# Kernel tuning notes

Measured on AMD Instinct MI355X. Metric: run time of the kernel, lower is better.

The kernel has to match this reference:

```python
import jax, jax.numpy as jnp
import numpy as np

N_NODES = 50000
N_EDGES = 500000
NODE_IN = 128
EDGE_IN = 64
HID = 128
OUT = 1


def _linear_params(key, fan_in, fan_out):
    # torch nn.Linear default init: U(-1/sqrt(fan_in), 1/sqrt(fan_in))
    kw, kb = jax.random.split(key)
    bound = 1.0 / np.sqrt(fan_in)
    W = jax.random.uniform(kw, (fan_in, fan_out), jnp.float32, -bound, bound)
    b = jax.random.uniform(kb, (fan_out,), jnp.float32, -bound, bound)
    return W, b


def setup_inputs() -> dict:
    key = jax.random.key(0)
    ks = jax.random.split(key, 8)
    x = jax.random.normal(ks[0], (N_NODES, NODE_IN), jnp.float32)
    edge_index = jax.random.randint(ks[1], (2, N_EDGES), 0, N_NODES, jnp.int64)
    edge_attr = jax.random.normal(ks[2], (N_EDGES, EDGE_IN), jnp.float32)
    Wn, bn = _linear_params(ks[3], NODE_IN, HID)
    We, be = _linear_params(ks[4], EDGE_IN, HID)
    W1, b1 = _linear_params(ks[5], HID * 3, HID * 4)
    W2, b2 = _linear_params(ks[6], HID * 4, HID * 2)
    W3, b3 = _linear_params(ks[7], HID * 2, OUT)
    return {
        "x": x, "edge_index": edge_index, "edge_attr": edge_attr,
        "Wn": Wn, "bn": bn, "We": We, "be": be,
        "W1": W1, "b1": b1, "W2": W2, "b2": b2, "W3": W3, "b3": b3,
    }


def reference(x, edge_index, edge_attr, Wn, bn, We, be, W1, b1, W2, b2, W3, b3):
    src, dst = edge_index[0], edge_index[1]
    node_f = jax.nn.relu(x @ Wn + bn)          # [N, H]
    edge_f = jax.nn.relu(edge_attr @ We + be)  # [E, H]
    combined = jnp.concatenate([node_f[src], node_f[dst], edge_f], axis=1)  # [E, 3H]
    h = jax.nn.relu(combined @ W1 + b1)        # [E, 4H]
    h = jax.nn.relu(h @ W2 + b2)               # [E, 2H]
    return h @ W3 + b3                          # [E, OUT]
```

## Files before the change

### kernel.cpp

```cpp
#include <hip/hip_runtime.h>
#include <hip/hip_bf16.h>
#include <stdint.h>

#define N_NODES 50000
#define N_EDGES 500000
#define NODE_IN 128
#define EDGE_IN 64
#define HID 128
#define K_H1 384
#define N_H1 512
#define N_H2 256

#define EPB 64

typedef short s8v __attribute__((ext_vector_type(8)));
typedef float f4v __attribute__((ext_vector_type(4)));

__device__ __forceinline__ unsigned int pk_bf16(float a, float b) {
    union { __hip_bfloat162 h; unsigned int u; } c;
    c.h = __float22bfloat162_rn(float2{a, b});
    return c.u;
}

__device__ __forceinline__ s8v load_a_f32(const float* __restrict__ base, int row, int ld, int koff) {
    const float4* p = (const float4*)(base + row * ld + koff);
    float4 x0 = p[0];
    float4 x1 = p[1];
    union { s8v v; unsigned int u[4]; } r;
    r.u[0] = pk_bf16(x0.x, x0.y);
    r.u[1] = pk_bf16(x0.z, x0.w);
    r.u[2] = pk_bf16(x1.x, x1.y);
    r.u[3] = pk_bf16(x1.z, x1.w);
    return r.v;
}

__device__ __forceinline__ void pack_one(const float* __restrict__ src, unsigned short* __restrict__ dst,
                                         int idx, int N) {
    int j = idx & 7;
    int lane = (idx >> 3) & 63;
    int rest = idx >> 9;
    int NT = N >> 4;
    int nt = rest % NT;
    int kb = rest / NT;
    int n = nt * 16 + (lane & 15);
    int k = kb * 32 + ((lane >> 4) << 3) + j;
    union { __hip_bfloat16 h; unsigned short s; } c;
    c.h = __float2bfloat16(src[k * N + n]);
    dst[idx] = c.s;
}

#define WN_ELEMS (NODE_IN * HID)
#define WE_ELEMS (EDGE_IN * HID)
#define W1_ELEMS (K_H1 * N_H1)
#define W2_ELEMS (N_H1 * N_H2)
#define PACK_TOTAL (WN_ELEMS + WE_ELEMS + W1_ELEMS + W2_ELEMS)

__global__ void pack_all(const float* __restrict__ Wn, const float* __restrict__ We,
                         const float* __restrict__ W1, const float* __restrict__ W2,
                         unsigned short* __restrict__ Wnp, unsigned short* __restrict__ Wep,
                         unsigned short* __restrict__ W1p, unsigned short* __restrict__ W2p) {
    int idx = blockIdx.x * blockDim.x + threadIdx.x;
    if (idx >= PACK_TOTAL) return;
    if (idx < WN_ELEMS) { pack_one(Wn, Wnp, idx, HID); return; }
    idx -= WN_ELEMS;
    if (idx < WE_ELEMS) { pack_one(We, Wep, idx, HID); return; }
    idx -= WE_ELEMS;
    if (idx < W1_ELEMS) { pack_one(W1, W1p, idx, N_H1); return; }
    idx -= W1_ELEMS;
    pack_one(W2, W2p, idx, N_H2);
}

__global__ __launch_bounds__(256, 4) void node_feat_kernel(
    const float* __restrict__ x, const unsigned short* __restrict__ Wnp,
    const float* __restrict__ bn, unsigned short* __restrict__ node_f)
{
    int tid = threadIdx.x;
    int wave = tid >> 6, lane = tid & 63;
    int lm = lane & 15, quad = lane >> 4;
    int row0 = blockIdx.x * 64;
    int node = row0 + wave * 16 + lm;
    int nodec = node < N_NODES ? node : N_NODES - 1;

    f4v zero = {0.f, 0.f, 0.f, 0.f};
    f4v acc[8];
    #pragma unroll
    for (int mt = 0; mt < 8; ++mt) acc[mt] = zero;

    for (int kb = 0; kb < 4; ++kb) {
        s8v b = load_a_f32(x, nodec, NODE_IN, kb * 32 + quad * 8);
        #pragma unroll
        for (int mt = 0; mt < 8; ++mt) {
            s8v a = *(const s8v*)(Wnp + (((kb * 8 + mt) * 64 + lane) << 3));
            acc[mt] = __builtin_amdgcn_mfma_f32_16x16x32_bf16(a, b, acc[mt], 0, 0, 0);
        }
    }

    if (node < N_NODES) {
        #pragma unroll
        for (int mt = 0; mt < 8; ++mt) {
            float4 bv = *(const float4*)(bn + mt * 16 + quad * 4);
            uint2 pk;
            pk.x = pk_bf16(fmaxf(acc[mt][0] + bv.x, 0.f), fmaxf(acc[mt][1] + bv.y, 0.f));
            pk.y = pk_bf16(fmaxf(acc[mt][2] + bv.z, 0.f), fmaxf(acc[mt][3] + bv.w, 0.f));
            *(uint2*)(node_f + node * HID + mt * 16 + quad * 4) = pk;
        }
    }
}

#define CSTR 392
#define H1STR 520

__global__ __launch_bounds__(512, 4) void fused_edge_kernel(
    const int* __restrict__ edge_index, const float* __restrict__ edge_attr,
    const unsigned short* __restrict__ node_f,
    const unsigned short* __restrict__ Wep, const float* __restrict__ be,
    const unsigned short* __restrict__ W1p, const float* __restrict__ b1,
    const unsigned short* __restrict__ W2p, const float* __restrict__ b2,
    const float* __restrict__ W3, const float* __restrict__ b3,
    float* __restrict__ out)
{
    __shared__ __align__(16) unsigned short smem[EPB * H1STR];
    __shared__ float out_lds[EPB];

    int tid = threadIdx.x;
    int wave = tid >> 6, lane = tid & 63;
    int lm = lane & 15, quad = lane >> 4;
    int e0 = blockIdx.x * EPB;

    if (tid < EPB) out_lds[tid] = 0.f;

    int gi = tid >> 3, gp = tid & 7;
    uint4 gs0, gs1, gd0, gd1;
    {
        int e = e0 + gi;
        int ec = e < N_EDGES ? e : N_EDGES - 1;
        int s = edge_index[ec];
        int d = edge_index[N_EDGES + ec];
        const uint4* ps = (const uint4*)(node_f + s * HID + gp * 16);
        const uint4* pd = (const uint4*)(node_f + d * HID + gp * 16);
        gs0 = ps[0]; gs1 = ps[1];
        gd0 = pd[0]; gd1 = pd[1];
    }

    {
        int nt = wave & 3;
        int mbase = (wave >> 2) * 4;
        int erow = e0 + nt * 16 + lm;
        if (erow >= N_EDGES) erow = N_EDGES - 1;

        f4v zero = {0.f, 0.f, 0.f, 0.f};
        f4v acc[4];
        #pragma unroll
        for (int t = 0; t < 4; ++t) acc[t] = zero;

        for (int kb = 0; kb < 2; ++kb) {
            s8v b = load_a_f32(edge_attr, erow, EDGE_IN, kb * 32 + quad * 8);
            #pragma unroll
            for (int t = 0; t < 4; ++t) {
                s8v a = *(const s8v*)(Wep + (((kb * 8 + mbase + t) * 64 + lane) << 3));
                acc[t] = __builtin_amdgcn_mfma_f32_16x16x32_bf16(a, b, acc[t], 0, 0, 0);
            }
        }
        {
            uint4* cs = (uint4*)(smem + gi * CSTR + gp * 16);
            uint4* cd = (uint4*)(smem + gi * CSTR + 128 + gp * 16);
            cs[0] = gs0; cs[1] = gs1;
            cd[0] = gd0; cd[1] = gd1;
        }
        int edge = nt * 16 + lm;
        #pragma unroll
        for (int t = 0; t < 4; ++t) {
            int col = (mbase + t) * 16 + quad * 4;
            float4 bv = *(const float4*)(be + col);
            uint2 pk;
            pk.x = pk_bf16(fmaxf(acc[t][0] + bv.x, 0.f), fmaxf(acc[t][1] + bv.y, 0.f));
            pk.y = pk_bf16(fmaxf(acc[t][2] + bv.z, 0.f), fmaxf(acc[t][3] + bv.w, 0.f));
            *(uint2*)(smem + edge * CSTR + 256 + col) = pk;
        }
    }
    __syncthreads();

    f4v zero = {0.f, 0.f, 0.f, 0.f};
    f4v acc1[4][4];
    #pragma unroll
    for (int t = 0; t < 4; ++t)
        #pragma unroll
        for (int nt = 0; nt < 4; ++nt) acc1[t][nt] = zero;

    for (int kb = 0; kb < 12; ++kb) {
        s8v bfr[4];
        #pragma unroll
        for (int nt = 0; nt < 4; ++nt)
            bfr[nt] = *(const s8v*)(smem + (nt * 16 + lm) * CSTR + kb * 32 + quad * 8);
        s8v afr[4];
        #pragma unroll
        for (int t = 0; t < 4; ++t)
            afr[t] = *(const s8v*)(W1p + (((kb * 32 + wave * 4 + t) * 64 + lane) << 3));
        #pragma unroll
        for (int t = 0; t < 4; ++t)
            #pragma unroll
            for (int nt = 0; nt < 4; ++nt)
                acc1[t][nt] = __builtin_amdgcn_mfma_f32_16x16x32_bf16(afr[t], bfr[nt], acc1[t][nt], 0, 0, 0);
    }
    __syncthreads();

    #pragma unroll
    for (int t = 0; t < 4; ++t) {
        int col = (wave * 4 + t) * 16 + quad * 4;
        float4 bv = *(const float4*)(b1 + col);
        #pragma unroll
        for (int nt = 0; nt < 4; ++nt) {
            int edge = nt * 16 + lm;
            uint2 pk;
            pk.x = pk_bf16(fmaxf(acc1[t][nt][0] + bv.x, 0.f), fmaxf(acc1[t][nt][1] + bv.y, 0.f));
            pk.y = pk_bf16(fmaxf(acc1[t][nt][2] + bv.z, 0.f), fmaxf(acc1[t][nt][3] + bv.w, 0.f));
            *(uint2*)(smem + edge * H1STR + col) = pk;
        }
    }
    __syncthreads();

    f4v acc2[2][4];
    #pragma unroll
    for (int t = 0; t < 2; ++t)
        #pragma unroll
        for (int nt = 0; nt < 4; ++nt) acc2[t][nt] = zero;

    for (int kb = 0; kb < 16; ++kb) {
        s8v bfr[4];
        #pragma unroll
        for (int nt = 0; nt < 4; ++nt)
            bfr[nt] = *(const s8v*)(smem + (nt * 16 + lm) * H1STR + kb * 32 + quad * 8);
        s8v afr[2];
        #pragma unroll
        for (int t = 0; t < 2; ++t)
            afr[t] = *(const s8v*)(W2p + (((kb * 16 + wave * 2 + t) * 64 + lane) << 3));
        #pragma unroll
        for (int t = 0; t < 2; ++t)
            #pragma unroll
            for (int nt = 0; nt < 4; ++nt)
                acc2[t][nt] = __builtin_amdgcn_mfma_f32_16x16x32_bf16(afr[t], bfr[nt], acc2[t][nt], 0, 0, 0);
    }

    {
        float4 b2v[2], w3v[2];
        #pragma unroll
        for (int t = 0; t < 2; ++t) {
            int col = (wave * 2 + t) * 16 + quad * 4;
            b2v[t] = *(const float4*)(b2 + col);
            w3v[t] = *(const float4*)(W3 + col);
        }
        #pragma unroll
        for (int nt = 0; nt < 4; ++nt) {
            float p = 0.f;
            #pragma unroll
            for (int t = 0; t < 2; ++t) {
                p += fmaxf(acc2[t][nt][0] + b2v[t].x, 0.f) * w3v[t].x;
                p += fmaxf(acc2[t][nt][1] + b2v[t].y, 0.f) * w3v[t].y;
                p += fmaxf(acc2[t][nt][2] + b2v[t].z, 0.f) * w3v[t].z;
                p += fmaxf(acc2[t][nt][3] + b2v[t].w, 0.f) * w3v[t].w;
            }
            p += __shfl_xor(p, 16);
            p += __shfl_xor(p, 32);
            if (quad == 0)
                atomicAdd(&out_lds[nt * 16 + lm], p);
        }
    }
    __syncthreads();

    if (tid < EPB) {
        int e = e0 + tid;
        if (e < N_EDGES) out[e] = out_lds[tid] + b3[0];
    }
}

extern "C" void kernel_launch(void* const* d_in, const int* in_sizes, int n_in,
                              void* d_out, int out_size, void* d_ws, size_t ws_size,
                              hipStream_t stream)
{
    const float* x          = (const float*)d_in[0];
    const int*   edge_index = (const int*)d_in[1];
    const float* edge_attr  = (const float*)d_in[2];
    const float* Wn = (const float*)d_in[3];
    const float* bn = (const float*)d_in[4];
    const float* We = (const float*)d_in[5];
    const float* be = (const float*)d_in[6];
    const float* W1 = (const float*)d_in[7];
    const float* b1 = (const float*)d_in[8];
    const float* W2 = (const float*)d_in[9];
    const float* b2 = (const float*)d_in[10];
    const float* W3 = (const float*)d_in[11];
    const float* b3 = (const float*)d_in[12];
    float* out = (float*)d_out;

    char* ws = (char*)d_ws;
    unsigned short* node_f = (unsigned short*)ws;
    unsigned short* Wnp = (unsigned short*)(ws + 12800000);
    unsigned short* Wep = (unsigned short*)(ws + 12832768);
    unsigned short* W1p = (unsigned short*)(ws + 12849152);
    unsigned short* W2p = (unsigned short*)(ws + 13242368);

    pack_all<<<(PACK_TOTAL + 255) / 256, 256, 0, stream>>>(Wn, We, W1, W2, Wnp, Wep, W1p, W2p);

    node_feat_kernel<<<(N_NODES + 63) / 64, 256, 0, stream>>>(x, Wnp, bn, node_f);

    fused_edge_kernel<<<(N_EDGES + EPB - 1) / EPB, 512, 0, stream>>>(
        edge_index, edge_attr, node_f, Wep, be, W1p, b1, W2p, b2, W3, b3, out);
}
```

Before: 604.7 us.

## Double-buffer W1/W2 fragment loads in registers with explicit waitcnt pipelining

The two MFMA GEMM loops in the fused edge kernel now prefetch the next k-step's weight fragments from global memory into alternating register sets while the current step's MFMAs run. Explicit s_waitcnt and sched_barrier calls control when loads must have landed. The point is to hide global-load latency of the packed weights behind matrix math instead of stalling each iteration. The last iteration prefetches past the end of each weight buffer, so the workspace is reordered to keep those over-reads inside allocated memory. This adds register pressure and relies on hand-written wait counts staying correct.

```diff
diff --git a/kernel.cpp b/kernel.cpp
--- a/kernel.cpp
+++ b/kernel.cpp
@@ -178,6 +178,12 @@
             *(uint2*)(smem + edge * CSTR + 256 + col) = pk;
         }
     }
+
+    const unsigned short* wb1 = W1p + (((wave * 4) * 64 + lane) << 3);
+    s8v aev[4], aod[4];
+    #pragma unroll
+    for (int t = 0; t < 4; ++t) aev[t] = *(const s8v*)(wb1 + t * 512);
+
     __syncthreads();
 
     f4v zero = {0.f, 0.f, 0.f, 0.f};
@@ -187,20 +193,41 @@
         #pragma unroll
         for (int nt = 0; nt < 4; ++nt) acc1[t][nt] = zero;
 
-    for (int kb = 0; kb < 12; ++kb) {
+    {
+        const unsigned short* brp = smem + lm * CSTR + quad * 8;
+        const unsigned short* wnext = wb1 + 16384;
+
         s8v bfr[4];
-        #pragma unroll
-        for (int nt = 0; nt < 4; ++nt)
-            bfr[nt] = *(const s8v*)(smem + (nt * 16 + lm) * CSTR + kb * 32 + quad * 8);
-        s8v afr[4];
-        #pragma unroll
-        for (int t = 0; t < 4; ++t)
-            afr[t] = *(const s8v*)(W1p + (((kb * 32 + wave * 4 + t) * 64 + lane) << 3));
-        #pragma unroll
-        for (int t = 0; t < 4; ++t)
+        #pragma unroll 1
+        for (int kb = 0; kb < 12; kb += 2) {
+            #pragma unroll
+            for (int t = 0; t < 4; ++t) aod[t] = *(const s8v*)(wnext + t * 512);
+            wnext += 16384;
             #pragma unroll
             for (int nt = 0; nt < 4; ++nt)
-                acc1[t][nt] = __builtin_amdgcn_mfma_f32_16x16x32_bf16(afr[t], bfr[nt], acc1[t][nt], 0, 0, 0);
+                bfr[nt] = *(const s8v*)(brp + nt * (16 * CSTR));
+            asm volatile("s_waitcnt vmcnt(4) lgkmcnt(0)" ::: "memory");
+            __builtin_amdgcn_sched_barrier(0);
+            #pragma unroll
+            for (int t = 0; t < 4; ++t)
+                #pragma unroll
+                for (int nt = 0; nt < 4; ++nt)
+                    acc1[t][nt] = __builtin_amdgcn_mfma_f32_16x16x32_bf16(aev[t], bfr[nt], acc1[t][nt], 0, 0, 0);
+            #pragma unroll
+            for (int t = 0; t < 4; ++t) aev[t] = *(const s8v*)(wnext + t * 512);
+            wnext += 16384;
+            #pragma unroll
+            for (int nt = 0; nt < 4; ++nt)
+                bfr[nt] = *(const s8v*)(brp + 32 + nt * (16 * CSTR));
+            asm volatile("s_waitcnt vmcnt(4) lgkmcnt(0)" ::: "memory");
+            __builtin_amdgcn_sched_barrier(0);
+            #pragma unroll
+            for (int t = 0; t < 4; ++t)
+                #pragma unroll
+                for (int nt = 0; nt < 4; ++nt)
+                    acc1[t][nt] = __builtin_amdgcn_mfma_f32_16x16x32_bf16(aod[t], bfr[nt], acc1[t][nt], 0, 0, 0);
+            brp += 64;
+        }
     }
     __syncthreads();
 
@@ -217,6 +244,12 @@
             *(uint2*)(smem + edge * H1STR + col) = pk;
         }
     }
+
+    const unsigned short* wb2 = W2p + (((wave * 2) * 64 + lane) << 3);
+    s8v a3ev[2], a3od[2];
+    a3ev[0] = *(const s8v*)(wb2);
+    a3ev[1] = *(const s8v*)(wb2 + 512);
+
     __syncthreads();
 
     f4v acc2[2][4];
@@ -225,20 +258,41 @@
         #pragma unroll
         for (int nt = 0; nt < 4; ++nt) acc2[t][nt] = zero;
 
-    for (int kb = 0; kb < 16; ++kb) {
+    {
+        const unsigned short* hrp = smem + lm * H1STR + quad * 8;
+        const unsigned short* wnext = wb2 + 8192;
+
         s8v bfr[4];
-        #pragma unroll
-        for (int nt = 0; nt < 4; ++nt)
-            bfr[nt] = *(const s8v*)(smem + (nt * 16 + lm) * H1STR + kb * 32 + quad * 8);
-        s8v afr[2];
-        #pragma unroll
-        for (int t = 0; t < 2; ++t)
-            afr[t] = *(const s8v*)(W2p + (((kb * 16 + wave * 2 + t) * 64 + lane) << 3));
-        #pragma unroll
-        for (int t = 0; t < 2; ++t)
+        #pragma unroll 1
+        for (int kb = 0; kb < 16; kb += 2) {
+            a3od[0] = *(const s8v*)(wnext);
+            a3od[1] = *(const s8v*)(wnext + 512);
+            wnext += 8192;
             #pragma unroll
             for (int nt = 0; nt < 4; ++nt)
-                acc2[t][nt] = __builtin_amdgcn_mfma_f32_16x16x32_bf16(afr[t], bfr[nt], acc2[t][nt], 0, 0, 0);
+                bfr[nt] = *(const s8v*)(hrp + nt * (16 * H1STR));
+            asm volatile("s_waitcnt vmcnt(2) lgkmcnt(0)" ::: "memory");
+            __builtin_amdgcn_sched_barrier(0);
+            #pragma unroll
+            for (int t = 0; t < 2; ++t)
+                #pragma unroll
+                for (int nt = 0; nt < 4; ++nt)
+                    acc2[t][nt] = __builtin_amdgcn_mfma_f32_16x16x32_bf16(a3ev[t], bfr[nt], acc2[t][nt], 0, 0, 0);
+            a3ev[0] = *(const s8v*)(wnext);
+            a3ev[1] = *(const s8v*)(wnext + 512);
+            wnext += 8192;
+            #pragma unroll
+            for (int nt = 0; nt < 4; ++nt)
+                bfr[nt] = *(const s8v*)(hrp + 32 + nt * (16 * H1STR));
+            asm volatile("s_waitcnt vmcnt(2) lgkmcnt(0)" ::: "memory");
+            __builtin_amdgcn_sched_barrier(0);
+            #pragma unroll
+            for (int t = 0; t < 2; ++t)
+                #pragma unroll
+                for (int nt = 0; nt < 4; ++nt)
+                    acc2[t][nt] = __builtin_amdgcn_mfma_f32_16x16x32_bf16(a3od[t], bfr[nt], acc2[t][nt], 0, 0, 0);
+            hrp += 64;
+        }
     }
 
     {
@@ -294,10 +348,10 @@
 
     char* ws = (char*)d_ws;
     unsigned short* node_f = (unsigned short*)ws;
-    unsigned short* Wnp = (unsigned short*)(ws + 12800000);
-    unsigned short* Wep = (unsigned short*)(ws + 12832768);
-    unsigned short* W1p = (unsigned short*)(ws + 12849152);
-    unsigned short* W2p = (unsigned short*)(ws + 13242368);
+    unsigned short* W1p = (unsigned short*)(ws + 12800000);
+    unsigned short* W2p = (unsigned short*)(ws + 13193216);
+    unsigned short* Wnp = (unsigned short*)(ws + 13455360);
+    unsigned short* Wep = (unsigned short*)(ws + 13488128);
 
     pack_all<<<(PACK_TOTAL + 255) / 256, 256, 0, stream>>>(Wn, We, W1, W2, Wnp, Wep, W1p, W2p);
 
```

After: 500.3 us. 1.21x faster.

## Switch edge MLP GEMMs to 32x32x16 MFMA with software-pipelined operand loads

Applied to the files above, without the earlier changes.

Repacks W1 and W2 into a 32x32 MFMA fragment layout and rewrites the two big edge-MLP GEMMs to use mfma_f32_32x32x16_bf16 tiles. The K loops are double-buffered: the next weight and LDS fragments are loaded while the current MFMAs run, using explicit waitcnt and sched_barrier. The first weight fragments are prefetched before each __syncthreads. The intent is fewer fragment loads per FLOP and better hiding of global and LDS latency. The price is hand-managed wait counts that are fragile, plus a different register footprint.

```diff
diff --git a/kernel.cpp b/kernel.cpp
--- a/kernel.cpp
+++ b/kernel.cpp
@@ -15,6 +15,7 @@
 
 typedef short s8v __attribute__((ext_vector_type(8)));
 typedef float f4v __attribute__((ext_vector_type(4)));
+typedef float f16v __attribute__((ext_vector_type(16)));
 
 __device__ __forceinline__ unsigned int pk_bf16(float a, float b) {
     union { __hip_bfloat162 h; unsigned int u; } c;
@@ -49,6 +50,21 @@
     dst[idx] = c.s;
 }
 
+__device__ __forceinline__ void pack_one32(const float* __restrict__ src, unsigned short* __restrict__ dst,
+                                           int idx, int N) {
+    int j = idx & 7;
+    int lane = (idx >> 3) & 63;
+    int rest = idx >> 9;
+    int NT = N >> 5;
+    int nt = rest % NT;
+    int ks = rest / NT;
+    int n = nt * 32 + (lane & 31);
+    int k = ks * 16 + ((lane >> 5) << 3) + j;
+    union { __hip_bfloat16 h; unsigned short s; } c;
+    c.h = __float2bfloat16(src[k * N + n]);
+    dst[idx] = c.s;
+}
+
 #define WN_ELEMS (NODE_IN * HID)
 #define WE_ELEMS (EDGE_IN * HID)
 #define W1_ELEMS (K_H1 * N_H1)
@@ -65,9 +81,9 @@
     idx -= WN_ELEMS;
     if (idx < WE_ELEMS) { pack_one(We, Wep, idx, HID); return; }
     idx -= WE_ELEMS;
-    if (idx < W1_ELEMS) { pack_one(W1, W1p, idx, N_H1); return; }
+    if (idx < W1_ELEMS) { pack_one32(W1, W1p, idx, N_H1); return; }
     idx -= W1_ELEMS;
-    pack_one(W2, W2p, idx, N_H2);
+    pack_one32(W2, W2p, idx, N_H2);
 }
 
 __global__ __launch_bounds__(256, 4) void node_feat_kernel(
@@ -125,6 +141,7 @@
     int tid = threadIdx.x;
     int wave = tid >> 6, lane = tid & 63;
     int lm = lane & 15, quad = lane >> 4;
+    int e32 = lane & 31, hi = lane >> 5;
     int e0 = blockIdx.x * EPB;
 
     if (tid < EPB) out_lds[tid] = 0.f;
@@ -148,10 +165,10 @@
         int erow = e0 + nt * 16 + lm;
         if (erow >= N_EDGES) erow = N_EDGES - 1;
 
-        f4v zero = {0.f, 0.f, 0.f, 0.f};
+        f4v zero4 = {0.f, 0.f, 0.f, 0.f};
         f4v acc[4];
         #pragma unroll
-        for (int t = 0; t < 4; ++t) acc[t] = zero;
+        for (int t = 0; t < 4; ++t) acc[t] = zero4;
 
         for (int kb = 0; kb < 2; ++kb) {
             s8v b = load_a_f32(edge_attr, erow, EDGE_IN, kb * 32 + quad * 8);
@@ -178,91 +195,151 @@
             *(uint2*)(smem + edge * CSTR + 256 + col) = pk;
         }
     }
+
+    const unsigned short* wb1 = W1p + (((wave * 2) * 64 + lane) << 3);
+    s8v aev[2], aod[2];
+    aev[0] = *(const s8v*)(wb1);
+    aev[1] = *(const s8v*)(wb1 + 512);
+
     __syncthreads();
 
-    f4v zero = {0.f, 0.f, 0.f, 0.f};
-    f4v acc1[4][4];
-    #pragma unroll
-    for (int t = 0; t < 4; ++t)
-        #pragma unroll
-        for (int nt = 0; nt < 4; ++nt) acc1[t][nt] = zero;
-
-    for (int kb = 0; kb < 12; ++kb) {
-        s8v bfr[4];
-        #pragma unroll
-        for (int nt = 0; nt < 4; ++nt)
-            bfr[nt] = *(const s8v*)(smem + (nt * 16 + lm) * CSTR + kb * 32 + quad * 8);
-        s8v afr[4];
-        #pragma unroll
-        for (int t = 0; t < 4; ++t)
-            afr[t] = *(const s8v*)(W1p + (((kb * 32 + wave * 4 + t) * 64 + lane) << 3));
-        #pragma unroll
-        for (int t = 0; t < 4; ++t)
-            #pragma unroll
-            for (int nt = 0; nt < 4; ++nt)
-                acc1[t][nt] = __builtin_amdgcn_mfma_f32_16x16x32_bf16(afr[t], bfr[nt], acc1[t][nt], 0, 0, 0);
-    }
-    __syncthreads();
-
-    #pragma unroll
-    for (int t = 0; t < 4; ++t) {
-        int col = (wave * 4 + t) * 16 + quad * 4;
-        float4 bv = *(const float4*)(b1 + col);
-        #pragma unroll
-        for (int nt = 0; nt < 4; ++nt) {
-            int edge = nt * 16 + lm;
-            uint2 pk;
-            pk.x = pk_bf16(fmaxf(acc1[t][nt][0] + bv.x, 0.f), fmaxf(acc1[t][nt][1] + bv.y, 0.f));
-            pk.y = pk_bf16(fmaxf(acc1[t][nt][2] + bv.z, 0.f), fmaxf(acc1[t][nt][3] + bv.w, 0.f));
-            *(uint2*)(smem + edge * H1STR + col) = pk;
-        }
-    }
-    __syncthreads();
-
-    f4v acc2[2][4];
+    f16v acc1[2][2];
     #pragma unroll
     for (int t = 0; t < 2; ++t)
         #pragma unroll
-        for (int nt = 0; nt < 4; ++nt) acc2[t][nt] = zero;
-
-    for (int kb = 0; kb < 16; ++kb) {
-        s8v bfr[4];
-        #pragma unroll
-        for (int nt = 0; nt < 4; ++nt)
-            bfr[nt] = *(const s8v*)(smem + (nt * 16 + lm) * H1STR + kb * 32 + quad * 8);
-        s8v afr[2];
-        #pragma unroll
-        for (int t = 0; t < 2; ++t)
-            afr[t] = *(const s8v*)(W2p + (((kb * 16 + wave * 2 + t) * 64 + lane) << 3));
-        #pragma unroll
-        for (int t = 0; t < 2; ++t)
-            #pragma unroll
-            for (int nt = 0; nt < 4; ++nt)
-                acc2[t][nt] = __builtin_amdgcn_mfma_f32_16x16x32_bf16(afr[t], bfr[nt], acc2[t][nt], 0, 0, 0);
-    }
-
-    {
-        float4 b2v[2], w3v[2];
+        for (int n = 0; n < 2; ++n)
+            acc1[t][n] = (f16v){0.f,0.f,0.f,0.f,0.f,0.f,0.f,0.f,
+                                0.f,0.f,0.f,0.f,0.f,0.f,0.f,0.f};
+
+    {
+        const unsigned short* brp = smem + e32 * CSTR + hi * 8;
+        s8v bev[2], bod[2];
+        bev[0] = *(const s8v*)(brp);
+        bev[1] = *(const s8v*)(brp + 32 * CSTR);
+
+        const unsigned short* wnx = wb1 + 8192;
+        const unsigned short* bnx = brp + 16;
+
+        #pragma unroll 1
+        for (int ks = 0; ks < 24; ks += 2) {
+            aod[0] = *(const s8v*)(wnx);
+            aod[1] = *(const s8v*)(wnx + 512);
+            wnx += 8192;
+            bod[0] = *(const s8v*)(bnx);
+            bod[1] = *(const s8v*)(bnx + 32 * CSTR);
+            bnx += 16;
+            asm volatile("s_waitcnt vmcnt(2) lgkmcnt(2)" ::: "memory");
+            __builtin_amdgcn_sched_barrier(0);
+            #pragma unroll
+            for (int t = 0; t < 2; ++t)
+                #pragma unroll
+                for (int n = 0; n < 2; ++n)
+                    acc1[t][n] = __builtin_amdgcn_mfma_f32_32x32x16_bf16(aev[t], bev[n], acc1[t][n], 0, 0, 0);
+            aev[0] = *(const s8v*)(wnx);
+            aev[1] = *(const s8v*)(wnx + 512);
+            wnx += 8192;
+            bev[0] = *(const s8v*)(bnx);
+            bev[1] = *(const s8v*)(bnx + 32 * CSTR);
+            bnx += 16;
+            asm volatile("s_waitcnt vmcnt(2) lgkmcnt(2)" ::: "memory");
+            __builtin_amdgcn_sched_barrier(0);
+            #pragma unroll
+            for (int t = 0; t < 2; ++t)
+                #pragma unroll
+                for (int n = 0; n < 2; ++n)
+                    acc1[t][n] = __builtin_amdgcn_mfma_f32_32x32x16_bf16(aod[t], bod[n], acc1[t][n], 0, 0, 0);
+        }
+    }
+    __syncthreads();
+
+    {
         #pragma unroll
         for (int t = 0; t < 2; ++t) {
-            int col = (wave * 2 + t) * 16 + quad * 4;
-            b2v[t] = *(const float4*)(b2 + col);
-            w3v[t] = *(const float4*)(W3 + col);
-        }
-        #pragma unroll
-        for (int nt = 0; nt < 4; ++nt) {
-            float p = 0.f;
-            #pragma unroll
-            for (int t = 0; t < 2; ++t) {
-                p += fmaxf(acc2[t][nt][0] + b2v[t].x, 0.f) * w3v[t].x;
-                p += fmaxf(acc2[t][nt][1] + b2v[t].y, 0.f) * w3v[t].y;
-                p += fmaxf(acc2[t][nt][2] + b2v[t].z, 0.f) * w3v[t].z;
-                p += fmaxf(acc2[t][nt][3] + b2v[t].w, 0.f) * w3v[t].w;
+            int mb = (wave * 2 + t) * 32 + 4 * hi;
+            #pragma unroll
+            for (int g = 0; g < 4; ++g) {
+                float4 bv = *(const float4*)(b1 + mb + g * 8);
+                #pragma unroll
+                for (int n = 0; n < 2; ++n) {
+                    int edge = n * 32 + e32;
+                    uint2 pk;
+                    pk.x = pk_bf16(fmaxf(acc1[t][n][4 * g + 0] + bv.x, 0.f),
+                                   fmaxf(acc1[t][n][4 * g + 1] + bv.y, 0.f));
+                    pk.y = pk_bf16(fmaxf(acc1[t][n][4 * g + 2] + bv.z, 0.f),
+                                   fmaxf(acc1[t][n][4 * g + 3] + bv.w, 0.f));
+                    *(uint2*)(smem + edge * H1STR + mb + g * 8) = pk;
+                }
             }
-            p += __shfl_xor(p, 16);
-            p += __shfl_xor(p, 32);
-            if (quad == 0)
-                atomicAdd(&out_lds[nt * 16 + lm], p);
+        }
+    }
+
+    const unsigned short* wb2 = W2p + ((wave * 64 + lane) << 3);
+    s8v a3ev, a3od;
+    a3ev = *(const s8v*)(wb2);
+
+    __syncthreads();
+
+    f16v acc2[2];
+    #pragma unroll
+    for (int n = 0; n < 2; ++n)
+        acc2[n] = (f16v){0.f,0.f,0.f,0.f,0.f,0.f,0.f,0.f,
+                         0.f,0.f,0.f,0.f,0.f,0.f,0.f,0.f};
+
+    {
+        const unsigned short* hrp = smem + e32 * H1STR + hi * 8;
+        s8v bev[2], bod[2];
+        bev[0] = *(const s8v*)(hrp);
+        bev[1] = *(const s8v*)(hrp + 32 * H1STR);
+
+        const unsigned short* wnx = wb2 + 4096;
+        const unsigned short* bnx = hrp + 16;
+
+        #pragma unroll 1
+        for (int ks = 0; ks < 32; ks += 2) {
+            a3od = *(const s8v*)(wnx);
+            wnx += 4096;
+            bod[0] = *(const s8v*)(bnx);
+            bod[1] = *(const s8v*)(bnx + 32 * H1STR);
+            bnx += 16;
+            asm volatile("s_waitcnt vmcnt(1) lgkmcnt(2)" ::: "memory");
+            __builtin_amdgcn_sched_barrier(0);
+            #pragma unroll
+            for (int n = 0; n < 2; ++n)
+                acc2[n] = __builtin_amdgcn_mfma_f32_32x32x16_bf16(a3ev, bev[n], acc2[n], 0, 0, 0);
+            a3ev = *(const s8v*)(wnx);
+            wnx += 4096;
+            bev[0] = *(const s8v*)(bnx);
+            bev[1] = *(const s8v*)(bnx + 32 * H1STR);
+            bnx += 16;
+            asm volatile("s_waitcnt vmcnt(1) lgkmcnt(2)" ::: "memory");
+            __builtin_amdgcn_sched_barrier(0);
+            #pragma unroll
+            for (int n = 0; n < 2; ++n)
+                acc2[n] = __builtin_amdgcn_mfma_f32_32x32x16_bf16(a3od, bod[n], acc2[n], 0, 0, 0);
+        }
+    }
+
+    {
+        int mb = wave * 32 + 4 * hi;
+        float p0 = 0.f, p1 = 0.f;
+        #pragma unroll
+        for (int g = 0; g < 4; ++g) {
+            float4 bv = *(const float4*)(b2 + mb + g * 8);
+            float4 wv = *(const float4*)(W3 + mb + g * 8);
+            p0 += fmaxf(acc2[0][4 * g + 0] + bv.x, 0.f) * wv.x;
+            p0 += fmaxf(acc2[0][4 * g + 1] + bv.y, 0.f) * wv.y;
+            p0 += fmaxf(acc2[0][4 * g + 2] + bv.z, 0.f) * wv.z;
+            p0 += fmaxf(acc2[0][4 * g + 3] + bv.w, 0.f) * wv.w;
+            p1 += fmaxf(acc2[1][4 * g + 0] + bv.x, 0.f) * wv.x;
+            p1 += fmaxf(acc2[1][4 * g + 1] + bv.y, 0.f) * wv.y;
+            p1 += fmaxf(acc2[1][4 * g + 2] + bv.z, 0.f) * wv.z;
+            p1 += fmaxf(acc2[1][4 * g + 3] + bv.w, 0.f) * wv.w;
+        }
+        p0 += __shfl_xor(p0, 32);
+        p1 += __shfl_xor(p1, 32);
+        if (hi == 0) {
+            atomicAdd(&out_lds[e32], p0);
+            atomicAdd(&out_lds[32 + e32], p1);
         }
     }
     __syncthreads();
@@ -294,10 +371,10 @@
 
     char* ws = (char*)d_ws;
     unsigned short* node_f = (unsigned short*)ws;
-    unsigned short* Wnp = (unsigned short*)(ws + 12800000);
-    unsigned short* Wep = (unsigned short*)(ws + 12832768);
-    unsigned short* W1p = (unsigned short*)(ws + 12849152);
-    unsigned short* W2p = (unsigned short*)(ws + 13242368);
+    unsigned short* W1p = (unsigned short*)(ws + 12800000);
+    unsigned short* W2p = (unsigned short*)(ws + 13193216);
+    unsigned short* Wnp = (unsigned short*)(ws + 13455360);
+    unsigned short* Wep = (unsigned short*)(ws + 13488128);
 
     pack_all<<<(PACK_TOTAL + 255) / 256, 256, 0, stream>>>(Wn, We, W1, W2, Wnp, Wep, W1p, W2p);
 
```

After: 538.2 us. 11.0% less time.
